# Kernel tuning notes

Hardware: AMD Instinct MI355X
Metric: run time of the kernel (lower is better)

Reference implementation:

```python
import jax, jax.numpy as jnp
import numpy as np


def setup_inputs() -> dict:
    key = jax.random.key(0)
    k1, k2 = jax.random.split(key)
    B, D, H, W, K = 64, 256, 32, 32, 1024
    x = jax.random.normal(k1, (B, D, H, W), dtype=jnp.float32)
    # codebook: torch.rand -> uniform [0,1), shape (emb_dim, num_emb)
    emb = jax.random.uniform(k2, (D, K), dtype=jnp.float32)
    return {"x": x, "emb": emb}


def reference(x, emb):
    # x: (B, D, H, W); emb: (D, K)
    B, D, H, W = x.shape
    K = emb.shape[1]
    # flatten latents: (N, D) with N = B*H*W (matches permute(0,2,3,1).view)
    xf = x.transpose(0, 2, 3, 1).reshape(-1, D)
    # (argmin of squared dist == argmin of L2 norm in the torch code)
    d2 = (
        jnp.sum(xf * xf, axis=1, keepdims=True)
        - 2.0 * (xf @ emb)
        + jnp.sum(emb * emb, axis=0)[None, :]
    )  # (N, K)
    argmin = jnp.argmin(d2, axis=1)  # (N,)
    q = jnp.take(emb.T, argmin, axis=0)  # (N, D) gather of nearest codes
    out = q.reshape(B, H, W, D).transpose(0, 3, 1, 2)  # back to (B, D, H, W)
    return out, argmin.reshape(B, H, W)
```

## Files before the change

kernel.cpp:

```cpp
#include <hip/hip_runtime.h>


typedef _Float16 half8 __attribute__((ext_vector_type(8)));
typedef float f32x4v __attribute__((ext_vector_type(4)));
typedef float f32x16 __attribute__((ext_vector_type(16)));
typedef const __attribute__((address_space(1))) unsigned int* gp_t;
typedef __attribute__((address_space(3))) unsigned int* lp_t;

#define K_DIM 1024
#define D_DIM 256

__global__ __launch_bounds__(256) void vq_prep(const float* __restrict__ emb,
                                               float* __restrict__ nhp,
                                               char* __restrict__ eimg_h,
                                               char* __restrict__ eimg_l) {
  __shared__ float tile[32][66];
  const int t = threadIdx.x;
  const int ki = blockIdx.x >> 3, di = blockIdx.x & 7;
  const int d0 = di * 32, k0 = ki * 64;
#pragma unroll
  for (int r = 0; r < 4; ++r) {
    int slot = r * 256 + t;
    int dr = slot >> 5, c2 = slot & 31;
    float2 v = *(const float2*)(emb + (size_t)(d0 + dr) * K_DIM + k0 + c2 * 2);
    *(float2*)&tile[dr][c2 * 2] = v;
  }
  __syncthreads();
  const int codeL = t >> 2, q = t & 3;
  half8 hh, ll;
  float s = 0.f;
#pragma unroll
  for (int j = 0; j < 8; ++j) {
    float v = tile[q * 8 + j][codeL];
    _Float16 h = (_Float16)v;
    hh[j] = h;
    ll[j] = (_Float16)(v - (float)h);
    s = fmaf(v, v, s);
  }
  const int dblk = di * 4 + q;
  const int phys = dblk ^ (codeL & 31);
  const size_t off = (size_t)ki * 32768 + codeL * 512 + phys * 16;
  *(half8*)(eimg_h + off) = hh;
  *(half8*)(eimg_l + off) = ll;
  s += __shfl_xor(s, 1);
  s += __shfl_xor(s, 2);
  if (q == 0) nhp[di * K_DIM + k0 + codeL] = s;
}

#define STAGE(tile_i, bufsel)                                                 \
  {                                                                           \
    const size_t tb = (size_t)(tile_i) * 32768 + t * 16;                      \
    _Pragma("unroll") for (int r = 0; r < 4; ++r) {                           \
      __builtin_amdgcn_global_load_lds((gp_t)(eimg_h + tb + r * 8192),        \
                                       (lp_t)(ebuf_h[bufsel] + t * 16 +       \
                                              r * 8192),                      \
                                       16, 0, 0);                             \
      __builtin_amdgcn_global_load_lds((gp_t)(eimg_l + tb + r * 8192),        \
                                       (lp_t)(ebuf_l[bufsel] + t * 16 +       \
                                              r * 8192),                      \
                                       16, 0, 0);                             \
    }                                                                         \
  }

#define XSTAGE(ci, xb_sel)                                                    \
  __builtin_amdgcn_global_load_lds(                                           \
      (gp_t)(xb + (size_t)((ci) * 8 + (t >> 6)) * K_DIM + (t & 63) * 4),      \
      (lp_t)((char*)x_lds + (xb_sel) * 8192 + t * 16), 16, 0, 0)

__global__ __launch_bounds__(512, 2) void vq_main(
    const float* __restrict__ x, const float* __restrict__ emb,
    const float* __restrict__ nhp, const char* __restrict__ eimg_h,
    const char* __restrict__ eimg_l, float* __restrict__ out,
    float* __restrict__ aout) {
  __shared__ __align__(16) char ebuf_h[2][32768];
  __shared__ __align__(16) char ebuf_l[2][32768];
  __shared__ __align__(16) float x_lds[2][8][256];
  __shared__ float nh_s[1024];
  __shared__ int bk_s[256];

  const int t = threadIdx.x;
  const int w = t >> 6, l = t & 63, lr = l & 31, lhi = l >> 5;
  const int b = blockIdx.x >> 2;
  const int hw0 = (blockIdx.x & 3) * 256;
  const float* xb = x + (size_t)b * D_DIM * K_DIM + hw0;
  const int myrow = w * 32 + lr;

#pragma unroll
  for (int i = 0; i < 2; ++i) {
    int c = i * 512 + t;
    float s = 0.f;
#pragma unroll
    for (int p = 0; p < 8; ++p) s += nhp[p * K_DIM + c];
    nh_s[c] = -0.5f * s;
  }

  STAGE(0, 0);
  XSTAGE(0, 0);

  half8 Bh[16], Bl[16];
#pragma unroll
  for (int ci = 0; ci < 32; ++ci) {
    __syncthreads();
    if (ci < 31) XSTAGE(ci + 1, (ci + 1) & 1);
    if (lhi == (ci & 1)) {
      const int ks = ci >> 1;
      half8 hv, lv;
#pragma unroll
      for (int j = 0; j < 8; ++j) {
        float v = x_lds[ci & 1][j][myrow];
        _Float16 h = (_Float16)v;
        hv[j] = h;
        lv[j] = (_Float16)(v - (float)h);
      }
      Bh[ks] = hv;
      Bl[ks] = lv;
    }
  }

  float bestv = -3.4e38f;
  int bestk = 0;

  for (int ti = 0; ti < 16; ++ti) {
    const int buf = ti & 1;
    if (ti < 15) STAGE(ti + 1, buf ^ 1);
    f32x16 acc[2];
#pragma unroll
    for (int Mt = 0; Mt < 2; ++Mt)
#pragma unroll
      for (int rg = 0; rg < 4; ++rg) {
        f32x4v nv = *(const f32x4v*)&nh_s[ti * 64 + Mt * 32 + rg * 8 + lhi * 4];
#pragma unroll
        for (int j = 0; j < 4; ++j) acc[Mt][rg * 4 + j] = nv[j];
      }
#pragma unroll
    for (int ks = 0; ks < 16; ++ks) {
      const int po = ((ks * 2 + lhi) ^ lr) * 16;
      half8 Ah0 = *(const half8*)(ebuf_h[buf] + lr * 512 + po);
      half8 Ah1 = *(const half8*)(ebuf_h[buf] + 16384 + lr * 512 + po);
      half8 Al0 = *(const half8*)(ebuf_l[buf] + lr * 512 + po);
      half8 Al1 = *(const half8*)(ebuf_l[buf] + 16384 + lr * 512 + po);
      __builtin_amdgcn_s_setprio(1);
      acc[0] = __builtin_amdgcn_mfma_f32_32x32x16_f16(Ah0, Bh[ks], acc[0], 0, 0, 0);
      acc[1] = __builtin_amdgcn_mfma_f32_32x32x16_f16(Ah1, Bh[ks], acc[1], 0, 0, 0);
      acc[0] = __builtin_amdgcn_mfma_f32_32x32x16_f16(Al0, Bh[ks], acc[0], 0, 0, 0);
      acc[1] = __builtin_amdgcn_mfma_f32_32x32x16_f16(Al1, Bh[ks], acc[1], 0, 0, 0);
      acc[0] = __builtin_amdgcn_mfma_f32_32x32x16_f16(Ah0, Bl[ks], acc[0], 0, 0, 0);
      acc[1] = __builtin_amdgcn_mfma_f32_32x32x16_f16(Ah1, Bl[ks], acc[1], 0, 0, 0);
      __builtin_amdgcn_s_setprio(0);
    }
#pragma unroll
    for (int Mt = 0; Mt < 2; ++Mt)
#pragma unroll
      for (int reg = 0; reg < 16; ++reg) {
        int code = ti * 64 + Mt * 32 + (reg & 3) + 8 * (reg >> 2) + 4 * lhi;
        float v = acc[Mt][reg];
        if (v > bestv || (v == bestv && code < bestk)) {
          bestv = v;
          bestk = code;
        }
      }
    __syncthreads();
  }

  {
    float ov = __shfl_xor(bestv, 32);
    int ok = __shfl_xor(bestk, 32);
    if (ov > bestv || (ov == bestv && ok < bestk)) {
      bestv = ov;
      bestk = ok;
    }
    if (lhi == 0) {
      bk_s[myrow] = bestk;
      aout[(size_t)blockIdx.x * 256 + myrow] = (float)bestk;
    }
  }
  __syncthreads();
  const int dgrp = t >> 6, n4 = (t & 63) * 4;
  const int kk0 = bk_s[n4], kk1 = bk_s[n4 + 1], kk2 = bk_s[n4 + 2],
            kk3 = bk_s[n4 + 3];
#pragma unroll 4
  for (int i = 0; i < 32; ++i) {
    int d = i * 8 + dgrp;
    const float* er = emb + (size_t)d * K_DIM;
    float4 v = {er[kk0], er[kk1], er[kk2], er[kk3]};
    *(float4*)(out + ((size_t)b * D_DIM + d) * K_DIM + hw0 + n4) = v;
  }
}

extern "C" void kernel_launch(void* const* d_in, const int* in_sizes, int n_in,
                              void* d_out, int out_size, void* d_ws,
                              size_t ws_size, hipStream_t stream) {
  const float* x = (const float*)d_in[0];
  const float* emb = (const float*)d_in[1];
  float* out = (float*)d_out;
  float* aout = out + (size_t)64 * 256 * 32 * 32;
  float* nhp = (float*)d_ws;
  char* eimg_h = (char*)d_ws + 32768;
  char* eimg_l = eimg_h + 524288;
  vq_prep<<<128, 256, 0, stream>>>(emb, nhp, eimg_h, eimg_l);
  vq_main<<<256, 512, 0, stream>>>(x, emb, nhp, eimg_h, eimg_l, out, aout);
}
```

Before: 235.0 us.

## Interleave codebook staging with MFMA phases and reuse ebuf for x prologue

Removes the separate x_lds buffer and stages x tiles into the unused second codebook buffer, using 4-deep buffering with explicit vmcnt waits. This halves the prologue iterations and cuts full __syncthreads. In the main loop, the next codebook tile's global->LDS loads are split into eight slices, one issued per two-k-step MFMA phase. Explicit s_barrier, waitcnt and sched_barrier calls replace the compiler-managed synchronisation. This overlaps memory traffic with matrix math and may free LDS for occupancy. In exchange it adds more barriers per tile and depends on fragile manual waitcnt ordering, which risks races.

```diff
diff --git a/kernel.cpp b/kernel.cpp
--- a/kernel.cpp
+++ b/kernel.cpp
@@ -9,6 +9,8 @@
 
 #define K_DIM 1024
 #define D_DIM 256
+
+#define MFMA32(A, B, C) __builtin_amdgcn_mfma_f32_32x32x16_f16(A, B, C, 0, 0, 0)
 
 __global__ __launch_bounds__(256) void vq_prep(const float* __restrict__ emb,
                                                float* __restrict__ nhp,
@@ -62,10 +64,37 @@
     }                                                                         \
   }
 
-#define XSTAGE(ci, xb_sel)                                                    \
-  __builtin_amdgcn_global_load_lds(                                           \
-      (gp_t)(xb + (size_t)((ci) * 8 + (t >> 6)) * K_DIM + (t & 63) * 4),      \
-      (lp_t)((char*)x_lds + (xb_sel) * 8192 + t * 16), 16, 0, 0)
+#define STAGE1(tile_i, bufsel, q)                                             \
+  {                                                                           \
+    const size_t tb = (size_t)(tile_i) * 32768 + t * 16;                      \
+    if ((q) < 4) {                                                            \
+      __builtin_amdgcn_global_load_lds((gp_t)(eimg_h + tb + (q) * 8192),      \
+                                       (lp_t)(ebuf_h[bufsel] + t * 16 +       \
+                                              (q) * 8192),                    \
+                                       16, 0, 0);                             \
+    } else {                                                                  \
+      __builtin_amdgcn_global_load_lds(                                       \
+          (gp_t)(eimg_l + tb + ((q) - 4) * 8192),                             \
+          (lp_t)(ebuf_l[bufsel] + t * 16 + ((q) - 4) * 8192), 16, 0, 0);      \
+    }                                                                         \
+  }
+
+#define XBUF(q) \
+  ((q) < 2 ? (ebuf_h[1] + (q) * 16384) : (ebuf_l[1] + ((q) - 2) * 16384))
+
+#define XSTAGE(ci, q)                                                         \
+  {                                                                           \
+    _Pragma("unroll") for (int r = 0; r < 2; ++r) {                           \
+      int slot = r * 512 + t;                                                 \
+      __builtin_amdgcn_global_load_lds(                                       \
+          (gp_t)(xb + (size_t)((ci) * 16 + (slot >> 6)) * K_DIM +             \
+                 (slot & 63) * 4),                                            \
+          (lp_t)(XBUF(q) + slot * 16), 16, 0, 0);                             \
+    }                                                                         \
+  }
+
+#define SBAR() __builtin_amdgcn_s_barrier()
+#define SCHED0() __builtin_amdgcn_sched_barrier(0)
 
 __global__ __launch_bounds__(512, 2) void vq_main(
     const float* __restrict__ x, const float* __restrict__ emb,
@@ -74,7 +103,6 @@
     float* __restrict__ aout) {
   __shared__ __align__(16) char ebuf_h[2][32768];
   __shared__ __align__(16) char ebuf_l[2][32768];
-  __shared__ __align__(16) float x_lds[2][8][256];
   __shared__ float nh_s[1024];
   __shared__ int bk_s[256];
 
@@ -94,27 +122,29 @@
     nh_s[c] = -0.5f * s;
   }
 
+  XSTAGE(0, 0);
+  XSTAGE(1, 1);
+  XSTAGE(2, 2);
   STAGE(0, 0);
-  XSTAGE(0, 0);
-
   half8 Bh[16], Bl[16];
 #pragma unroll
-  for (int ci = 0; ci < 32; ++ci) {
-    __syncthreads();
-    if (ci < 31) XSTAGE(ci + 1, (ci + 1) & 1);
-    if (lhi == (ci & 1)) {
-      const int ks = ci >> 1;
-      half8 hv, lv;
-#pragma unroll
-      for (int j = 0; j < 8; ++j) {
-        float v = x_lds[ci & 1][j][myrow];
-        _Float16 h = (_Float16)v;
-        hv[j] = h;
-        lv[j] = (_Float16)(v - (float)h);
-      }
-      Bh[ks] = hv;
-      Bl[ks] = lv;
-    }
+  for (int ci = 0; ci < 16; ++ci) {
+    asm volatile("s_waitcnt vmcnt(4)" ::: "memory");
+    SCHED0();
+    SBAR();
+    SCHED0();
+    if (ci + 3 < 16) XSTAGE(ci + 3, (ci + 3) & 3);
+    const float* xsf = (const float*)XBUF(ci & 3);
+    half8 hv, lv;
+#pragma unroll
+    for (int j = 0; j < 8; ++j) {
+      float v = xsf[(lhi * 8 + j) * 256 + myrow];
+      _Float16 h = (_Float16)v;
+      hv[j] = h;
+      lv[j] = (_Float16)(v - (float)h);
+    }
+    Bh[ci] = hv;
+    Bl[ci] = lv;
   }
 
   float bestv = -3.4e38f;
@@ -122,7 +152,13 @@
 
   for (int ti = 0; ti < 16; ++ti) {
     const int buf = ti & 1;
-    if (ti < 15) STAGE(ti + 1, buf ^ 1);
+    asm volatile("s_waitcnt vmcnt(0)" ::: "memory");
+    SCHED0();
+    SBAR();
+    SCHED0();
+    const char* bh0 = ebuf_h[buf];
+    const char* bl0 = ebuf_l[buf];
+    const int tn = (ti + 1) & 15;
     f32x16 acc[2];
 #pragma unroll
     for (int Mt = 0; Mt < 2; ++Mt)
@@ -133,20 +169,38 @@
         for (int j = 0; j < 4; ++j) acc[Mt][rg * 4 + j] = nv[j];
       }
 #pragma unroll
-    for (int ks = 0; ks < 16; ++ks) {
-      const int po = ((ks * 2 + lhi) ^ lr) * 16;
-      half8 Ah0 = *(const half8*)(ebuf_h[buf] + lr * 512 + po);
-      half8 Ah1 = *(const half8*)(ebuf_h[buf] + 16384 + lr * 512 + po);
-      half8 Al0 = *(const half8*)(ebuf_l[buf] + lr * 512 + po);
-      half8 Al1 = *(const half8*)(ebuf_l[buf] + 16384 + lr * 512 + po);
+    for (int ph = 0; ph < 8; ++ph) {
+      const int ks0 = ph * 2, ks1 = ph * 2 + 1;
+      const int poa = ((ks0 * 2 + lhi) ^ lr) * 16;
+      const int pob = ((ks1 * 2 + lhi) ^ lr) * 16;
+      half8 Ah0a = *(const half8*)(bh0 + lr * 512 + poa);
+      half8 Ah1a = *(const half8*)(bh0 + 16384 + lr * 512 + poa);
+      half8 Al0a = *(const half8*)(bl0 + lr * 512 + poa);
+      half8 Al1a = *(const half8*)(bl0 + 16384 + lr * 512 + poa);
+      half8 Ah0b = *(const half8*)(bh0 + lr * 512 + pob);
+      half8 Ah1b = *(const half8*)(bh0 + 16384 + lr * 512 + pob);
+      half8 Al0b = *(const half8*)(bl0 + lr * 512 + pob);
+      half8 Al1b = *(const half8*)(bl0 + 16384 + lr * 512 + pob);
+      STAGE1(tn, buf ^ 1, ph);
+      SBAR();
+      asm volatile("s_waitcnt lgkmcnt(0)" ::: "memory");
+      SCHED0();
       __builtin_amdgcn_s_setprio(1);
-      acc[0] = __builtin_amdgcn_mfma_f32_32x32x16_f16(Ah0, Bh[ks], acc[0], 0, 0, 0);
-      acc[1] = __builtin_amdgcn_mfma_f32_32x32x16_f16(Ah1, Bh[ks], acc[1], 0, 0, 0);
-      acc[0] = __builtin_amdgcn_mfma_f32_32x32x16_f16(Al0, Bh[ks], acc[0], 0, 0, 0);
-      acc[1] = __builtin_amdgcn_mfma_f32_32x32x16_f16(Al1, Bh[ks], acc[1], 0, 0, 0);
-      acc[0] = __builtin_amdgcn_mfma_f32_32x32x16_f16(Ah0, Bl[ks], acc[0], 0, 0, 0);
-      acc[1] = __builtin_amdgcn_mfma_f32_32x32x16_f16(Ah1, Bl[ks], acc[1], 0, 0, 0);
+      acc[0] = MFMA32(Ah0a, Bh[ks0], acc[0]);
+      acc[1] = MFMA32(Ah1a, Bh[ks0], acc[1]);
+      acc[0] = MFMA32(Al0a, Bh[ks0], acc[0]);
+      acc[1] = MFMA32(Al1a, Bh[ks0], acc[1]);
+      acc[0] = MFMA32(Ah0a, Bl[ks0], acc[0]);
+      acc[1] = MFMA32(Ah1a, Bl[ks0], acc[1]);
+      acc[0] = MFMA32(Ah0b, Bh[ks1], acc[0]);
+      acc[1] = MFMA32(Ah1b, Bh[ks1], acc[1]);
+      acc[0] = MFMA32(Al0b, Bh[ks1], acc[0]);
+      acc[1] = MFMA32(Al1b, Bh[ks1], acc[1]);
+      acc[0] = MFMA32(Ah0b, Bl[ks1], acc[0]);
+      acc[1] = MFMA32(Ah1b, Bl[ks1], acc[1]);
       __builtin_amdgcn_s_setprio(0);
+      SCHED0();
+      SBAR();
     }
 #pragma unroll
     for (int Mt = 0; Mt < 2; ++Mt)
@@ -159,7 +213,6 @@
           bestk = code;
         }
       }
-    __syncthreads();
   }
 
   {
```

After: 226.6 us. 3.6% less time.
